# Optimization experiments

Hardware: AMD Instinct MI355X
Metric: run time of the kernel (lower is better)

## Reference

```python
import jax, jax.numpy as jnp
import numpy as np

EMBED_DIM = 256
NUM_HEADS = 8
HEAD_DIM = EMBED_DIM // NUM_HEADS
NUM_POINTS_LIST = [4, 4, 4, 4]
PT = sum(NUM_POINTS_LIST)  # 16 points per head, total_points = 8*16 = 128
OFFSET_SCALE = 0.5
SHAPES = np.array([[128, 128], [64, 64], [32, 32], [16, 16]], dtype=np.int32)
BS, LQ = 8, 1000


def setup_inputs() -> dict:
    key = jax.random.key(0)
    ks = jax.random.split(key, 12)
    Lv = int((SHAPES[:, 0] * SHAPES[:, 1]).sum())  # 21760
    C = EMBED_DIM
    s = 0.02
    return {
        "query": jax.random.normal(ks[0], (BS, LQ, C), jnp.float32),
        "reference_points": jax.random.uniform(ks[1], (BS, LQ, 1, 4), jnp.float32, 0.1, 0.9),
        "value": jax.random.normal(ks[2], (BS, Lv, C), jnp.float32),
        "spatial_shapes": SHAPES,  # static numpy, not traced
        "w_off": jax.random.normal(ks[3], (C, NUM_HEADS * PT * 2), jnp.float32) * s,
        "b_off": jax.random.normal(ks[4], (NUM_HEADS * PT * 2,), jnp.float32) * 0.5,
        "w_attn": jax.random.normal(ks[5], (C, NUM_HEADS * PT), jnp.float32) * s,
        "b_attn": jnp.zeros((NUM_HEADS * PT,), jnp.float32),
        "w_val": jax.random.normal(ks[6], (C, C), jnp.float32) * s,
        "b_val": jnp.zeros((C,), jnp.float32),
        "w_out": jax.random.normal(ks[7], (C, C), jnp.float32) * s,
        "b_out": jnp.zeros((C,), jnp.float32),
    }


def _sample_level(v, loc, H, W):
    """Bilinear sample (grid_sample, align_corners=False, zero padding).
    v:   [bs, nH, H*W, hd]  value features of one pyramid level
    loc: [bs, Lq, nH, P, 2] sampling locations in [0,1] (x, y)
    returns [bs, Lq, nH, P, hd]
    """
    bs, Lq, nH, P, _ = loc.shape
    hd = v.shape[-1]
    x = loc[..., 0] * W - 0.5
    y = loc[..., 1] * H - 0.5
    x0 = jnp.floor(x)
    y0 = jnp.floor(y)
    lx = x - x0
    ly = y - y0
    x0i = x0.astype(jnp.int32)
    y0i = y0.astype(jnp.int32)

    def corner(xi, yi, w):
        valid = (xi >= 0) & (xi < W) & (yi >= 0) & (yi < H)
        idx = jnp.clip(yi, 0, H - 1) * W + jnp.clip(xi, 0, W - 1)  # [bs,Lq,nH,P]
        idxf = jnp.transpose(idx, (0, 2, 1, 3)).reshape(bs, nH, Lq * P)
        g = jnp.take_along_axis(v, idxf[..., None], axis=2)  # [bs,nH,Lq*P,hd]
        wv = jnp.where(valid, w, 0.0).astype(v.dtype)
        wf = jnp.transpose(wv, (0, 2, 1, 3)).reshape(bs, nH, Lq * P, 1)
        return g * wf

    out = (corner(x0i, y0i, (1 - lx) * (1 - ly))
           + corner(x0i + 1, y0i, lx * (1 - ly))
           + corner(x0i, y0i + 1, (1 - lx) * ly)
           + corner(x0i + 1, y0i + 1, lx * ly))
    out = out.reshape(bs, nH, Lq, P, hd)
    return jnp.transpose(out, (0, 2, 1, 3, 4))


def reference(query, reference_points, value, spatial_shapes,
              w_off, b_off, w_attn, b_attn, w_val, b_val, w_out, b_out):
    shapes = np.asarray(spatial_shapes)  # static
    bs, Lq, C = query.shape
    Lv = value.shape[1]
    nH, hd, Pt = NUM_HEADS, HEAD_DIM, PT

    # value projection -> [bs, nH, Lv, hd]
    v = value @ w_val + b_val
    v = jnp.transpose(v.reshape(bs, Lv, nH, hd), (0, 2, 1, 3))

    # sampling offsets and attention weights from query
    off = (query @ w_off + b_off).reshape(bs, Lq, nH, Pt, 2)
    aw = jax.nn.softmax((query @ w_attn + b_attn).reshape(bs, Lq, nH, Pt), axis=-1)

    # reference_points: [bs, Lq, 1, 4] boxes (cx, cy, w, h) in [0,1]
    nps = jnp.asarray([1.0 / n for n in NUM_POINTS_LIST for _ in range(n)],
                      dtype=query.dtype)[:, None]  # [Pt,1]
    loc = (reference_points[:, :, None, :, :2]
           + off * nps * reference_points[:, :, None, :, 2:] * OFFSET_SCALE)  # [bs,Lq,nH,Pt,2]

    samples = []
    v_start = 0
    p_start = 0
    for l, (H, W) in enumerate(shapes):
        H, W = int(H), int(W)
        P = NUM_POINTS_LIST[l]
        v_l = jax.lax.dynamic_slice_in_dim(v, v_start, H * W, axis=2)
        loc_l = loc[:, :, :, p_start:p_start + P, :]
        samples.append(_sample_level(v_l, loc_l, H, W))
        v_start += H * W
        p_start += P
    samples = jnp.concatenate(samples, axis=3)  # [bs,Lq,nH,Pt,hd]

    out = jnp.einsum('blhp,blhpd->blhd', aw, samples).reshape(bs, Lq, C)
    return out @ w_out + b_out
```

## Files before the change

kernel.cpp:

```cpp
#include <hip/hip_runtime.h>

typedef unsigned short ushort_t;
typedef short s16x8 __attribute__((ext_vector_type(8)));
typedef float f32x4 __attribute__((ext_vector_type(4)));
typedef unsigned int uint2_t __attribute__((ext_vector_type(2)));
typedef unsigned int uint4_t __attribute__((ext_vector_type(4)));

#define KDIM 256
#define BK 64
#define LDST 72
#define LV_TOTAL 21760
#define HL 696320
#define NQ 8000
#define VM_TILES_FB 680
#define QOA_BLOCKS 96
#define VPROJ_BLOCKS 320

__device__ inline unsigned short f2b(float f) {
  union { float f; unsigned u; } v; v.f = f;
  return (unsigned short)((v.u + 0x7fffu + ((v.u >> 16) & 1u)) >> 16);
}
__device__ inline float b2f(unsigned short h) {
  union { unsigned u; float f; } v; v.u = ((unsigned)h) << 16;
  return v.f;
}
__device__ inline unsigned pack_bf16x2(float lo, float hi) {
  union { float f; unsigned u; } a, b;
  a.f = lo; b.f = hi;
  return __builtin_amdgcn_perm(b.u + 0x8000u, a.u + 0x8000u, 0x07060302u);
}
__device__ inline unsigned short f2b_cheap(float f) {
  union { float f; unsigned u; } v; v.f = f;
  return (unsigned short)((v.u + 0x8000u) >> 16);
}

__global__ __launch_bounds__(256) void prep_weights(
    const float* __restrict__ w_off, const float* __restrict__ w_attn,
    const float* __restrict__ w_val, const float* __restrict__ w_out,
    const float* __restrict__ b_off, const float* __restrict__ b_attn,
    ushort_t* __restrict__ wt_val, ushort_t* __restrict__ wt_qoa,
    ushort_t* __restrict__ wt_out, float* __restrict__ bias_qoa,
    int* __restrict__ counters)
{
  int bid = blockIdx.x;
  int k = threadIdx.x;
  if (bid < 256) {
    int n = bid;
    wt_val[n*KDIM + k] = f2b(w_val[k*256 + n]);
  } else if (bid < 640) {
    int n = bid - 256;
    float v = (n < 256) ? w_off[k*256 + n] : w_attn[k*128 + (n - 256)];
    wt_qoa[n*KDIM + k] = f2b(v);
  } else if (bid < 896) {
    int n = bid - 640;
    wt_out[n*KDIM + k] = f2b(w_out[k*256 + n]);
  } else {
    if (k < 128) counters[k] = 0;
    for (int i = k; i < 384; i += 256)
      bias_qoa[i] = (i < 256) ? b_off[i] : b_attn[i - 256];
  }
}

__global__ __launch_bounds__(512, 2) void merged_gemms(
    const float* __restrict__ value, const ushort_t* __restrict__ wt_val,
    const float* __restrict__ b_val, ushort_t* __restrict__ v_proj,
    const float* __restrict__ query, const ushort_t* __restrict__ wt_qoa,
    const float* __restrict__ bias_qoa, float* __restrict__ qoa,
    int* __restrict__ counters)
{
  extern __shared__ __align__(16) char smem[];
  __shared__ int s_mt;
  const int tid  = threadIdx.x;
  const int wave = tid >> 6;
  const int lane = tid & 63;
  const int lrow = lane & 15;
  const int quad = lane >> 4;

  if (blockIdx.x < QOA_BLOCKS) {
    ushort_t* sA = (ushort_t*)smem;
    ushort_t* sB = (ushort_t*)(smem + 256 * LDST * 2);
    const int m0 = (blockIdx.x % 32) * 256;
    const int n0 = (blockIdx.x / 32) * 128;
    const int M = NQ, N = 384;

    f32x4 acc[2][8];
    #pragma unroll
    for (int i = 0; i < 2; ++i)
      #pragma unroll
      for (int j = 0; j < 8; ++j) acc[i][j] = {0.f, 0.f, 0.f, 0.f};

    for (int kc = 0; kc < KDIM; kc += BK) {
      #pragma unroll
      for (int i = 0; i < 8; ++i) {
        int f   = tid + i * 512;
        int row = f >> 4;
        int c4  = f & 15;
        int gr  = m0 + row;
        float4 val = {0.f, 0.f, 0.f, 0.f};
        if (gr < M) val = *(const float4*)(query + (size_t)gr * KDIM + kc + c4 * 4);
        uint2_t t;
        t.x = pack_bf16x2(val.x, val.y);
        t.y = pack_bf16x2(val.z, val.w);
        *(uint2_t*)&sA[row * LDST + c4 * 4] = t;
      }
      #pragma unroll
      for (int i = 0; i < 2; ++i) {
        int f   = tid + i * 512;
        int row = f >> 3;
        int seg = f & 7;
        s16x8 v = *(const s16x8*)(wt_qoa + (size_t)(n0 + row) * KDIM + kc + seg * 8);
        *(s16x8*)&sB[row * LDST + seg * 8] = v;
      }
      __syncthreads();
      #pragma unroll
      for (int ki = 0; ki < BK; ki += 32) {
        int krow = ki + quad * 8;
        s16x8 af[2], bfr[8];
        #pragma unroll
        for (int mt = 0; mt < 2; ++mt)
          af[mt] = *(const s16x8*)&sA[(wave * 32 + mt * 16 + lrow) * LDST + krow];
        #pragma unroll
        for (int nt = 0; nt < 8; ++nt)
          bfr[nt] = *(const s16x8*)&sB[(nt * 16 + lrow) * LDST + krow];
        #pragma unroll
        for (int mt = 0; mt < 2; ++mt)
          #pragma unroll
          for (int nt = 0; nt < 8; ++nt)
            acc[mt][nt] = __builtin_amdgcn_mfma_f32_16x16x32_bf16(
                bfr[nt], af[mt], acc[mt][nt], 0, 0, 0);
      }
      __syncthreads();
    }
    #pragma unroll
    for (int mt = 0; mt < 2; ++mt) {
      const int gm = m0 + wave * 32 + mt * 16 + lrow;
      if (gm < M) {
        #pragma unroll
        for (int nt = 0; nt < 8; ++nt) {
          const int gn = n0 + nt * 16 + quad * 4;
          const float4 b4 = *(const float4*)(bias_qoa + gn);
          float4 o = {acc[mt][nt][0] + b4.x, acc[mt][nt][1] + b4.y,
                      acc[mt][nt][2] + b4.z, acc[mt][nt][3] + b4.w};
          *(float4*)(qoa + (size_t)gm * N + gn) = o;
        }
      }
    }
    return;
  }

  ushort_t* sB = (ushort_t*)smem;

  {
    #pragma unroll
    for (int i = 0; i < 16; ++i) {
      int g   = tid + i * 512;
      int row = g >> 5;
      int c   = g & 31;
      s16x8 v = *(const s16x8*)(wt_val + (size_t)row * KDIM + c * 8);
      *(s16x8*)&sB[row * 256 + ((c ^ (row & 7)) * 8)] = v;
    }
  }
  __syncthreads();

  float bv[16];
  #pragma unroll
  for (int nt = 0; nt < 16; ++nt) bv[nt] = b_val[nt * 16 + lrow];

  const int swz = lrow & 7;

  while (true) {
    if (tid == 0) s_mt = atomicAdd(&counters[0], 1);
    __syncthreads();
    const int mt = s_mt;
    if (mt >= VM_TILES_FB) break;
    const int m0 = mt * 256;
    const int bidx  = mt / 85;
    const int rbase = m0 - bidx * 21760;
    const float* arow0 = value + (size_t)(m0 + wave * 32 + lrow) * KDIM + quad * 8;
    const float* arow1 = arow0 + 16 * KDIM;

    f32x4 acc[2][16];
    #pragma unroll
    for (int m = 0; m < 2; ++m)
      #pragma unroll
      for (int nt = 0; nt < 16; ++nt) acc[m][nt] = {0.f, 0.f, 0.f, 0.f};

    float4 st[2][2][2];
    st[0][0][0] = *(const float4*)(arow0);
    st[0][0][1] = *(const float4*)(arow0 + 4);
    st[0][1][0] = *(const float4*)(arow1);
    st[0][1][1] = *(const float4*)(arow1 + 4);

    #pragma unroll
    for (int ks = 0; ks < 8; ++ks) {
      const int cur = ks & 1, nxt = cur ^ 1;
      if (ks < 7) {
        const float* p0 = arow0 + (ks + 1) * 32;
        const float* p1 = arow1 + (ks + 1) * 32;
        st[nxt][0][0] = *(const float4*)(p0);
        st[nxt][0][1] = *(const float4*)(p0 + 4);
        st[nxt][1][0] = *(const float4*)(p1);
        st[nxt][1][1] = *(const float4*)(p1 + 4);
      }
      s16x8 af[2];
      #pragma unroll
      for (int m = 0; m < 2; ++m) {
        union { uint4_t d; s16x8 v; } u;
        u.d.x = pack_bf16x2(st[cur][m][0].x, st[cur][m][0].y);
        u.d.y = pack_bf16x2(st[cur][m][0].z, st[cur][m][0].w);
        u.d.z = pack_bf16x2(st[cur][m][1].x, st[cur][m][1].y);
        u.d.w = pack_bf16x2(st[cur][m][1].z, st[cur][m][1].w);
        af[m] = u.v;
      }
      #pragma unroll
      for (int nt = 0; nt < 16; ++nt) {
        s16x8 bf = *(const s16x8*)&sB[(nt * 16 + lrow) * 256 +
                                      (((4 * ks + quad) ^ swz) * 8)];
        acc[0][nt] = __builtin_amdgcn_mfma_f32_16x16x32_bf16(af[0], bf, acc[0][nt], 0, 0, 0);
        acc[1][nt] = __builtin_amdgcn_mfma_f32_16x16x32_bf16(af[1], bf, acc[1][nt], 0, 0, 0);
      }
    }

    #pragma unroll
    for (int m = 0; m < 2; ++m) {
      int rl = rbase + wave * 32 + m * 16 + quad * 4;
      #pragma unroll
      for (int nt = 0; nt < 16; ++nt) {
        int gn = nt * 16 + lrow;
        int h  = gn >> 5;
        int d  = gn & 31;
        ushort_t* dst = v_proj + (size_t)(bidx * 8 + h) * HL + (size_t)rl * 32 + d;
        #pragma unroll
        for (int r = 0; r < 4; ++r)
          dst[r * 32] = f2b_cheap(acc[m][nt][r] + bv[nt]);
      }
    }
    __syncthreads();
  }
}

__global__ __launch_bounds__(256) void ms_deform_sample(
    const ushort_t* __restrict__ v,
    const float* __restrict__ qoa,
    const float* __restrict__ refp,
    float* __restrict__ outq)
{
  __shared__ float s_w[4][512];
  __shared__ int   s_i[4][512];
  const int tid  = threadIdx.x;
  const int wave = tid >> 6;
  const int l    = tid & 63;
  const int bq   = blockIdx.x * 4 + wave;
  const int b    = bq / 1000;

  const float* qrow = qoa + (size_t)bq * 384;
  const float* rp   = refp + (size_t)bq * 4;
  const float rx = rp[0], ry = rp[1], rw = rp[2], rh = rp[3];

  {
    const int p   = l & 15;
    const int lvl = p >> 2;
    const int HWs[4] = {128, 64, 32, 16};
    const int STs[4] = {0, 16384, 20480, 21504};
    const int W = HWs[lvl], H = HWs[lvl], st = STs[lvl];

    float lg0 = qrow[256 + l];
    float lg1 = qrow[256 + 64 + l];
    float m0 = lg0, m1 = lg1;
    #pragma unroll
    for (int s = 8; s >= 1; s >>= 1) {
      m0 = fmaxf(m0, __shfl_xor(m0, s));
      m1 = fmaxf(m1, __shfl_xor(m1, s));
    }
    float e0 = __expf(lg0 - m0), e1 = __expf(lg1 - m1);
    float su0 = e0, su1 = e1;
    #pragma unroll
    for (int s = 8; s >= 1; s >>= 1) {
      su0 += __shfl_xor(su0, s);
      su1 += __shfl_xor(su1, s);
    }
    const float aw0 = e0 / su0, aw1 = e1 / su1;

    #pragma unroll
    for (int half = 0; half < 2; ++half) {
      const int s = l + half * 64;
      const float aw = half ? aw1 : aw0;
      const float ox = qrow[2 * s], oy = qrow[2 * s + 1];
      float x = (rx + ox * 0.125f * rw) * (float)W - 0.5f;
      float y = (ry + oy * 0.125f * rh) * (float)H - 0.5f;
      float x0f = floorf(x), y0f = floorf(y);
      int x0 = (int)x0f, y0 = (int)y0f;
      float fx = x - x0f, fy = y - y0f;
      float wc[4] = {(1.f - fx) * (1.f - fy), fx * (1.f - fy),
                     (1.f - fx) * fy,         fx * fy};
      #pragma unroll
      for (int c = 0; c < 4; ++c) {
        int xi = x0 + (c & 1);
        int yi = y0 + (c >> 1);
        bool valid = (xi >= 0) && (xi < W) && (yi >= 0) && (yi < H);
        int xc = min(max(xi, 0), W - 1);
        int yc = min(max(yi, 0), H - 1);
        s_w[wave][s * 4 + c] = valid ? wc[c] * aw : 0.f;
        s_i[wave][s * 4 + c] = st + yc * W + xc;
      }
    }
  }
  asm volatile("s_waitcnt lgkmcnt(0)" ::: "memory");

  const int h     = l >> 3;
  const int sub   = (l >> 1) & 3;
  const int cpair = l & 1;
  const ushort_t* vb = v + (size_t)(b * 8 + h) * HL + sub * 8;

  float acc[8];
  #pragma unroll
  for (int d = 0; d < 8; ++d) acc[d] = 0.f;

  #pragma unroll
  for (int batch = 0; batch < 4; ++batch) {
    float wgt[8]; int idx[8];
    #pragma unroll
    for (int u = 0; u < 8; ++u) {
      const int slot = batch * 8 + u;
      const int p  = slot >> 1;
      const int c  = cpair * 2 + (slot & 1);
      const int j  = h * 64 + p * 4 + c;
      wgt[u] = s_w[wave][j];
      idx[u] = s_i[wave][j];
    }
    s16x8 vv[8];
    #pragma unroll
    for (int u = 0; u < 8; ++u)
      vv[u] = *(const s16x8*)(vb + (size_t)idx[u] * 32);
    #pragma unroll
    for (int u = 0; u < 8; ++u)
      #pragma unroll
      for (int d = 0; d < 8; ++d)
        acc[d] += wgt[u] * b2f((ushort_t)vv[u][d]);
  }

  #pragma unroll
  for (int d = 0; d < 8; ++d) acc[d] += __shfl_xor(acc[d], 1);

  if (cpair == 0) {
    float* dst = outq + (size_t)bq * 256 + h * 32 + sub * 8;
    float4 o0 = {acc[0], acc[1], acc[2], acc[3]};
    float4 o1 = {acc[4], acc[5], acc[6], acc[7]};
    *(float4*)dst = o0;
    *(float4*)(dst + 4) = o1;
  }
}

__global__ __launch_bounds__(256) void gemm_bf16(
    const float* __restrict__ A, const ushort_t* __restrict__ Bt,
    const float* __restrict__ bias, float* __restrict__ Cf,
    int M, int N)
{
  __shared__ ushort_t sA[64 * LDST];
  __shared__ ushort_t sB[64 * LDST];
  const int tid  = threadIdx.x;
  const int m0   = blockIdx.x * 64;
  const int n0   = blockIdx.y * 64;
  const int wave = tid >> 6;
  const int lane = tid & 63;
  const int lrow = lane & 15;
  const int quad = lane >> 4;

  f32x4 acc[4];
  #pragma unroll
  for (int j = 0; j < 4; ++j) acc[j] = {0.f, 0.f, 0.f, 0.f};

  for (int kc = 0; kc < KDIM; kc += BK) {
    #pragma unroll
    for (int i = 0; i < 4; ++i) {
      int f   = tid + i * 256;
      int row = f >> 4;
      int c4  = f & 15;
      float4 val = *(const float4*)(A + (size_t)(m0 + row) * KDIM + kc + c4 * 4);
      uint2_t t;
      t.x = pack_bf16x2(val.x, val.y);
      t.y = pack_bf16x2(val.z, val.w);
      *(uint2_t*)&sA[row * LDST + c4 * 4] = t;
    }
    #pragma unroll
    for (int i = 0; i < 2; ++i) {
      int f   = tid + i * 256;
      int row = f >> 3;
      int seg = f & 7;
      s16x8 v = *(const s16x8*)(Bt + (size_t)(n0 + row) * KDIM + kc + seg * 8);
      *(s16x8*)&sB[row * LDST + seg * 8] = v;
    }
    __syncthreads();
    #pragma unroll
    for (int ki = 0; ki < BK; ki += 32) {
      int krow = ki + quad * 8;
      s16x8 af = *(const s16x8*)&sA[(wave * 16 + lrow) * LDST + krow];
      s16x8 bfr[4];
      #pragma unroll
      for (int nt = 0; nt < 4; ++nt)
        bfr[nt] = *(const s16x8*)&sB[(nt * 16 + lrow) * LDST + krow];
      #pragma unroll
      for (int nt = 0; nt < 4; ++nt)
        acc[nt] = __builtin_amdgcn_mfma_f32_16x16x32_bf16(bfr[nt], af, acc[nt], 0, 0, 0);
    }
    __syncthreads();
  }
  {
    const int gm = m0 + wave * 16 + lrow;
    #pragma unroll
    for (int nt = 0; nt < 4; ++nt) {
      const int gn = n0 + nt * 16 + quad * 4;
      const float4 b4 = *(const float4*)(bias + gn);
      float4 o = {acc[nt][0] + b4.x, acc[nt][1] + b4.y,
                  acc[nt][2] + b4.z, acc[nt][3] + b4.w};
      *(float4*)(Cf + (size_t)gm * N + gn) = o;
    }
  }
}

extern "C" void kernel_launch(void* const* d_in, const int* in_sizes, int n_in,
                              void* d_out, int out_size, void* d_ws, size_t ws_size,
                              hipStream_t stream) {
  const float* query  = (const float*)d_in[0];
  const float* refp   = (const float*)d_in[1];
  const float* value  = (const float*)d_in[2];
  const float* w_off  = (const float*)d_in[4];
  const float* b_off  = (const float*)d_in[5];
  const float* w_attn = (const float*)d_in[6];
  const float* b_attn = (const float*)d_in[7];
  const float* w_val  = (const float*)d_in[8];
  const float* b_val  = (const float*)d_in[9];
  const float* w_out  = (const float*)d_in[10];
  const float* b_out  = (const float*)d_in[11];
  float* out = (float*)d_out;

  char* ws = (char*)d_ws;
  const size_t WS_NEEDED = 110069760;
  if (ws_size < WS_NEEDED) return;
  ushort_t* wt_val   = (ushort_t*)(ws);
  ushort_t* wt_qoa   = (ushort_t*)(ws + 131072);
  ushort_t* wt_out   = (ushort_t*)(ws + 327680);
  float*    bias_qoa = (float*)   (ws + 458752);
  int*      counters = (int*)     (ws + 460288);
  ushort_t* v_proj   = (ushort_t*)(ws + 460800);
  float*    qoa      = (float*)   (ws + 89589760);
  float*    outq     = (float*)   (ws + 101877760);

  (void)hipFuncSetAttribute((const void*)merged_gemms,
                            hipFuncAttributeMaxDynamicSharedMemorySize, 131072);

  prep_weights<<<897, 256, 0, stream>>>(w_off, w_attn, w_val, w_out, b_off, b_attn,
                                        wt_val, wt_qoa, wt_out, bias_qoa, counters);
  merged_gemms<<<QOA_BLOCKS + VPROJ_BLOCKS, 512, 131072, stream>>>(
      value, wt_val, b_val, v_proj, query, wt_qoa, bias_qoa, qoa, counters);
  ms_deform_sample<<<NQ / 4, 256, 0, stream>>>(v_proj, qoa, refp, outq);
  gemm_bf16<<<dim3(125, 4), 256, 0, stream>>>(outq, wt_out, b_out, out, NQ, 256);
}
```

Measured before the change: 340.8 us.

## Schedule value-projection work per wave in 32-row strips with cross-strip prefetch

The value-projection GEMM loop now hands out work per wave rather than per block. Each wave claims 32-row strips through a lane-0 atomic plus readfirstlane, which removes the block-wide __syncthreads and the shared tile index. The A-operand prefetch is deepened to a 4-slot register ring two k-steps ahead, and it loads the next strip's first k-slices during the tail of the current strip, hiding global latency across strip boundaries. This is meant to cut barrier stalls and load bubbles, at the cost of more atomics and more registers for the larger staging buffer.

```diff
diff --git a/kernel.cpp b/kernel.cpp
--- a/kernel.cpp
+++ b/kernel.cpp
@@ -12,7 +12,7 @@
 #define LV_TOTAL 21760
 #define HL 696320
 #define NQ 8000
-#define VM_TILES_FB 680
+#define NSTRIPS_FB 5440
 #define QOA_BLOCKS 96
 #define VPROJ_BLOCKS 320
 
@@ -69,7 +69,6 @@
     int* __restrict__ counters)
 {
   extern __shared__ __align__(16) char smem[];
-  __shared__ int s_mt;
   const int tid  = threadIdx.x;
   const int wave = tid >> 6;
   const int lane = tid & 63;
@@ -168,16 +167,31 @@
 
   const int swz = lrow & 7;
 
-  while (true) {
-    if (tid == 0) s_mt = atomicAdd(&counters[0], 1);
-    __syncthreads();
-    const int mt = s_mt;
-    if (mt >= VM_TILES_FB) break;
-    const int m0 = mt * 256;
-    const int bidx  = mt / 85;
+  float4 st[4][2][2];
+
+#define LOADK(BUF, MM0, KK) do {                                              \
+    const float* _p = value + (size_t)((MM0) + lrow) * KDIM + (KK) * 32 + quad * 8; \
+    st[BUF][0][0] = *(const float4*)(_p);                                     \
+    st[BUF][0][1] = *(const float4*)(_p + 4);                                 \
+    st[BUF][1][0] = *(const float4*)(_p + 16 * KDIM);                         \
+    st[BUF][1][1] = *(const float4*)(_p + 16 * KDIM + 4);                     \
+  } while (0)
+
+  int s;
+  {
+    int t = 0;
+    if (lane == 0) t = atomicAdd(&counters[0], 1);
+    s = __builtin_amdgcn_readfirstlane(t);
+  }
+  if (s < NSTRIPS_FB) { LOADK(0, s * 32, 0); LOADK(1, s * 32, 1); }
+
+  while (s < NSTRIPS_FB) {
+    int tnext = 0;
+    if (lane == 0) tnext = atomicAdd(&counters[0], 1);
+
+    const int m0    = s * 32;
+    const int bidx  = s / 680;
     const int rbase = m0 - bidx * 21760;
-    const float* arow0 = value + (size_t)(m0 + wave * 32 + lrow) * KDIM + quad * 8;
-    const float* arow1 = arow0 + 16 * KDIM;
 
     f32x4 acc[2][16];
     #pragma unroll
@@ -185,31 +199,23 @@
       #pragma unroll
       for (int nt = 0; nt < 16; ++nt) acc[m][nt] = {0.f, 0.f, 0.f, 0.f};
 
-    float4 st[2][2][2];
-    st[0][0][0] = *(const float4*)(arow0);
-    st[0][0][1] = *(const float4*)(arow0 + 4);
-    st[0][1][0] = *(const float4*)(arow1);
-    st[0][1][1] = *(const float4*)(arow1 + 4);
-
+    int snext = NSTRIPS_FB;
     #pragma unroll
     for (int ks = 0; ks < 8; ++ks) {
-      const int cur = ks & 1, nxt = cur ^ 1;
-      if (ks < 7) {
-        const float* p0 = arow0 + (ks + 1) * 32;
-        const float* p1 = arow1 + (ks + 1) * 32;
-        st[nxt][0][0] = *(const float4*)(p0);
-        st[nxt][0][1] = *(const float4*)(p0 + 4);
-        st[nxt][1][0] = *(const float4*)(p1);
-        st[nxt][1][1] = *(const float4*)(p1 + 4);
+      if (ks == 6) snext = __builtin_amdgcn_readfirstlane(tnext);
+      if (ks < 6) {
+        LOADK((ks + 2) & 3, m0, ks + 2);
+      } else if (snext < NSTRIPS_FB) {
+        LOADK((ks + 2) & 3, snext * 32, ks - 6);
       }
       s16x8 af[2];
       #pragma unroll
       for (int m = 0; m < 2; ++m) {
         union { uint4_t d; s16x8 v; } u;
-        u.d.x = pack_bf16x2(st[cur][m][0].x, st[cur][m][0].y);
-        u.d.y = pack_bf16x2(st[cur][m][0].z, st[cur][m][0].w);
-        u.d.z = pack_bf16x2(st[cur][m][1].x, st[cur][m][1].y);
-        u.d.w = pack_bf16x2(st[cur][m][1].z, st[cur][m][1].w);
+        u.d.x = pack_bf16x2(st[ks & 3][m][0].x, st[ks & 3][m][0].y);
+        u.d.y = pack_bf16x2(st[ks & 3][m][0].z, st[ks & 3][m][0].w);
+        u.d.z = pack_bf16x2(st[ks & 3][m][1].x, st[ks & 3][m][1].y);
+        u.d.w = pack_bf16x2(st[ks & 3][m][1].z, st[ks & 3][m][1].w);
         af[m] = u.v;
       }
       #pragma unroll
@@ -223,7 +229,7 @@
 
     #pragma unroll
     for (int m = 0; m < 2; ++m) {
-      int rl = rbase + wave * 32 + m * 16 + quad * 4;
+      int rl = rbase + m * 16 + quad * 4;
       #pragma unroll
       for (int nt = 0; nt < 16; ++nt) {
         int gn = nt * 16 + lrow;
@@ -235,8 +241,9 @@
           dst[r * 32] = f2b_cheap(acc[m][nt][r] + bv[nt]);
       }
     }
-    __syncthreads();
-  }
+    s = snext;
+  }
+#undef LOADK
 }
 
 __global__ __launch_bounds__(256) void ms_deform_sample(
```

Measured after the change: 379.9 us. 1.11x slower.
